# Optimization experiments

Measured on AMD Instinct MI355X. Metric: run time of the kernel, lower is better.

Reference implementation:

```python
import jax, jax.numpy as jnp
import numpy as np

NUM_LAYER = 5
N_HIDDEN = 1024
EMB_SIZE = 1024
N_CLASS = 32000
BATCH = 64
SEQ = 256


def setup_inputs() -> dict:
    key = jax.random.key(0)
    ks = jax.random.split(key, 7)
    scale = 0.02
    X = jax.random.randint(ks[0], (BATCH, SEQ), 0, N_CLASS)
    emb = jax.random.normal(ks[1], (N_CLASS, EMB_SIZE), jnp.float32) * scale
    # gate order: [i, f, o, c_tilda]; layer 0 input dim == EMB_SIZE == N_HIDDEN
    Wx = jax.random.normal(ks[2], (NUM_LAYER, 4, N_HIDDEN, N_HIDDEN), jnp.float32) * scale
    Wh = jax.random.normal(ks[3], (NUM_LAYER, 4, N_HIDDEN, N_HIDDEN), jnp.float32) * scale
    b = jnp.ones((NUM_LAYER, 4, N_HIDDEN), jnp.float32)  # original inits gate biases to ones
    W_hq = jax.random.normal(ks[4], (N_HIDDEN, N_CLASS), jnp.float32) * scale
    b_q = jnp.ones((N_CLASS,), jnp.float32)
    return {"X": X, "emb": emb, "Wx": Wx, "Wh": Wh, "b": b, "W_hq": W_hq, "b_q": b_q}


def _lstm_stack(seq, Wx, Wh, b):
    # seq: [S, B, E] time-major input
    inp = seq
    for l in range(Wx.shape[0]):  # fixed small layer count
        # precompute input-to-gate projections for all timesteps: [S, 4, B, H]
        xp = jnp.einsum('sbe,geh->sgbh', inp, Wx[l]) + b[l][:, None, :]

        def step(carry, xp_t):
            h, c = carry
            pre = xp_t + jnp.einsum('bk,gkh->gbh', h, Wh[l])  # [4, B, H]
            i = jax.nn.sigmoid(pre[0])
            f = jax.nn.sigmoid(pre[1])
            o = jax.nn.sigmoid(pre[2])
            g = jnp.tanh(pre[3])
            c = f * c + i * g
            h = o * jnp.tanh(c)
            return (h, c), h

        h0 = jnp.zeros((seq.shape[1], Wh.shape[-1]), seq.dtype)
        (_, _), hs = jax.lax.scan(step, (h0, h0), xp)
        inp = hs  # [S, B, H] feeds next layer
    return inp


def reference(X, emb, Wx, Wh, b, W_hq, b_q):
    seq = emb[X].transpose(1, 0, 2)  # [S, B, E]
    hs = _lstm_stack(seq, Wx, Wh, b)
    # output projection on the final timestep's hidden state of the top layer
    return hs[-1] @ W_hq + b_q  # [B, N_CLASS]
```

## Files before the change

kernel.cpp:

```cpp
#include <hip/hip_runtime.h>

#define SEQL 256
#define BATCH 64
#define HID 1024
#define NLAY 5
#define NCLS 32000

typedef __attribute__((__ext_vector_type__(8))) short s16x8;
typedef __attribute__((__ext_vector_type__(4))) float f32x4;

__device__ __forceinline__ unsigned short f2bf(float f) {
  unsigned u = __float_as_uint(f);
  u = u + 0x7fffu + ((u >> 16) & 1u);
  return (unsigned short)(u >> 16);
}
__device__ __forceinline__ float bf2f(unsigned short s) {
  return __uint_as_float(((unsigned)s) << 16);
}
__device__ __forceinline__ float sigm(float x) { return 1.f / (1.f + __expf(-x)); }
__device__ __forceinline__ float tanh_f(float x) {
  float a = fabsf(x);
  float e = __expf(-2.f * a);
  float t = (1.f - e) / (1.f + e);
  return x < 0.f ? -t : t;
}

__device__ __forceinline__ void llds16(const void* g, void* l) {
  __builtin_amdgcn_global_load_lds((const __attribute__((address_space(1))) unsigned int*)g,
                                   (__attribute__((address_space(3))) unsigned int*)l,
                                   16, 0, 0);
}

#define AFENCE asm volatile("" ::: "memory")
#define VW0 asm volatile("s_waitcnt vmcnt(0)" ::: "memory")
#define LW0 asm volatile("s_waitcnt lgkmcnt(0)" ::: "memory")
#define SBAR __builtin_amdgcn_s_barrier()

__global__ void pack_k(const float* __restrict__ Wx, const float* __restrict__ Wh,
                       unsigned short* __restrict__ Wp) {
  int bid = blockIdx.x;
  int k0 = bid & 63;
  int g = (bid >> 6) & 3;
  int j = (bid >> 8) & 63;
  int l = bid >> 14;
  int lane = threadIdx.x;
  int h = j * 16 + (lane & 15);
  int kb = k0 * 32 + (lane >> 4) * 8;
  const float* src;
  if (kb < 1024) src = Wx + ((size_t)((l * 4 + g) * 1024 + kb)) * 1024 + h;
  else           src = Wh + ((size_t)((l * 4 + g) * 1024 + (kb - 1024))) * 1024 + h;
  unsigned short o[8];
#pragma unroll
  for (int i = 0; i < 8; ++i) o[i] = f2bf(src[(size_t)i * 1024]);
  uint4 v;
  v.x = (unsigned)o[0] | ((unsigned)o[1] << 16);
  v.y = (unsigned)o[2] | ((unsigned)o[3] << 16);
  v.z = (unsigned)o[4] | ((unsigned)o[5] << 16);
  v.w = (unsigned)o[6] | ((unsigned)o[7] << 16);
  *(uint4*)(Wp + (((size_t)bid * 64 + lane) * 8)) = v;
}

__global__ void embed_k(const int* __restrict__ X, const float* __restrict__ emb,
                        unsigned short* __restrict__ hsA) {
  int sb = blockIdx.x;
  int t = sb >> 6, b = sb & 63;
  int row = X[b * SEQL + t];
  float4 v = ((const float4*)(emb + (size_t)row * HID))[threadIdx.x];
  unsigned short o0 = f2bf(v.x), o1 = f2bf(v.y), o2 = f2bf(v.z), o3 = f2bf(v.w);
  uint2 pk;
  pk.x = (unsigned)o0 | ((unsigned)o1 << 16);
  pk.y = (unsigned)o2 | ((unsigned)o3 << 16);
  ((uint2*)(hsA + (size_t)sb * HID))[threadIdx.x] = pk;
}

extern __shared__ char smem[];

__device__ __forceinline__ void stage16(const char* slab, char* lbuf, int srow, int sslot) {
#pragma unroll
  for (int r = 0; r < 4; ++r) {
    int rw = r * 4 + srow;
    llds16(slab + rw * 2048 + ((sslot ^ (rw & 7)) << 4), lbuf + rw * 2048 + sslot * 16);
  }
}

__device__ __forceinline__ void pollflags(const int* fl, int id, int lane) {
  if (id <= 0) return;
  for (;;) {
    int v = __hip_atomic_load(&fl[lane * 4], __ATOMIC_RELAXED, __HIP_MEMORY_SCOPE_AGENT);
    if (__all(v >= id)) break;
    __builtin_amdgcn_s_sleep(1);
  }
}

__global__ void __launch_bounds__(512, 1)
lstm_pers(const unsigned short* __restrict__ Wp, const float* __restrict__ bias,
          unsigned short* hsA, unsigned short* hsB, int* flags) {
  const int bid = blockIdx.x;
  const int bg = bid >> 6;
  const int cg = bid & 63;
  const int tid = threadIdx.x;
  const int wave = tid >> 6;
  const int lane = tid & 63;
  const int g = wave & 3;
  const int kh = wave >> 2;
  const int hl = lane & 15;
  const int ksub = lane >> 4;
  const int srow = tid >> 7;
  const int sslot = tid & 127;

  char* Bx0 = smem;
  char* Bx1 = smem + 32768;
  char* Bh = smem + 65536;
  float* pre0 = (float*)(smem + 98304);
  float* pre1 = (float*)(smem + 102656);

  int* flbg = flags + bg * 256;

  for (int l = 0; l < NLAY; ++l) {
    const unsigned short* hin = (l & 1) ? hsB : hsA;
    unsigned short* hout = (l & 1) ? hsA : hsB;
    const unsigned short* wpL =
        Wp + (size_t)(l * 64 + cg) * 131072 + (size_t)g * 32768 + (size_t)kh * 32 * 512;
    const float biasv = bias[(l * 4 + g) * 1024 + cg * 16 + hl];

    s16x8 wreg[32];
#pragma unroll
    for (int i = 0; i < 32; ++i)
      wreg[i] = *(const s16x8*)(wpL + i * 512 + lane * 8);

    float c0 = 0.f, c1 = 0.f;

    if (wave == 4) pollflags(flbg, l * 256, lane);
    AFENCE; SBAR;
#pragma unroll
    for (int r = 0; r < 4; ++r)
      ((uint4*)Bh)[r * 512 + tid] = (uint4){0u, 0u, 0u, 0u};
    stage16((const char*)hin + (size_t)(bg * 16) * 2048, Bx0, srow, sslot);
    VW0; LW0; SBAR;

    for (int t = 0; t < SEQL; ++t) {
      char* Bxp = (t & 1) ? Bx1 : Bx0;
      char* Bxn = (t & 1) ? Bx0 : Bx1;
      const bool pre_ = (t + 1 < SEQL);

      if (pre_) {
        const char* xn = (const char*)hin + ((size_t)(t + 1) * 64 + bg * 16) * 2048;
        stage16(xn, Bxn, srow, sslot);
      }

      f32x4 acc = {0.f, 0.f, 0.f, 0.f};
      if (kh == 0) {
#pragma unroll
        for (int i = 0; i < 32; ++i) {
          int off = hl * 2048 + (((i * 4 + ksub) ^ (hl & 7)) << 4);
          s16x8 a = *(const s16x8*)(Bxp + off);
          acc = __builtin_amdgcn_mfma_f32_16x16x32_bf16(a, wreg[i], acc, 0, 0, 0);
        }
#pragma unroll
        for (int r = 0; r < 4; ++r)
          pre0[(g * 16 + ksub * 4 + r) * 17 + hl] = acc[r] + biasv;
      } else if (wave == 4 && t > 0) {
        pollflags(flbg, l * 256 + t, lane);
      }
      AFENCE; SBAR;

      if (t > 0) {
        const char* hp = (const char*)hout + ((size_t)(t - 1) * 64 + bg * 16) * 2048;
        stage16(hp, Bh, srow, sslot);
      }
      VW0; SBAR;

      if (kh == 1) {
#pragma unroll
        for (int i = 0; i < 32; ++i) {
          int off = hl * 2048 + (((i * 4 + ksub) ^ (hl & 7)) << 4);
          s16x8 a = *(const s16x8*)(Bh + off);
          acc = __builtin_amdgcn_mfma_f32_16x16x32_bf16(a, wreg[i], acc, 0, 0, 0);
        }
#pragma unroll
        for (int r = 0; r < 4; ++r)
          pre1[(g * 16 + ksub * 4 + r) * 17 + hl] = acc[r];
      }
      LW0; SBAR;

      if (tid < 128) {
        int b = tid >> 3;
        int h0 = (tid & 7) * 2;
        unsigned short hw[2];
#pragma unroll
        for (int q = 0; q < 2; ++q) {
          int hh = h0 + q;
          float pi = pre0[(0 * 16 + b) * 17 + hh] + pre1[(0 * 16 + b) * 17 + hh];
          float pf = pre0[(1 * 16 + b) * 17 + hh] + pre1[(1 * 16 + b) * 17 + hh];
          float po = pre0[(2 * 16 + b) * 17 + hh] + pre1[(2 * 16 + b) * 17 + hh];
          float pg = pre0[(3 * 16 + b) * 17 + hh] + pre1[(3 * 16 + b) * 17 + hh];
          float iv = sigm(pi), fv = sigm(pf), ov = sigm(po), gv = tanh_f(pg);
          float cprev = q ? c1 : c0;
          float c = fv * cprev + iv * gv;
          if (q) c1 = c; else c0 = c;
          hw[q] = f2bf(ov * tanh_f(c));
        }
        unsigned pk = (unsigned)hw[0] | ((unsigned)hw[1] << 16);
        unsigned* dst =
            (unsigned*)(hout + ((size_t)t * 64 + bg * 16 + b) * HID + cg * 16 + h0);
        __hip_atomic_store(dst, pk, __ATOMIC_RELAXED, __HIP_MEMORY_SCOPE_AGENT);
      }
      VW0;
      SBAR;
      if (tid == 0)
        __hip_atomic_store(&flags[(bg * 64 + cg) * 4], l * 256 + t + 1, __ATOMIC_RELAXED,
                           __HIP_MEMORY_SCOPE_AGENT);
    }
  }
}

__global__ void __launch_bounds__(256) proj_k(const unsigned short* __restrict__ hlast,
                                              const float* __restrict__ Whq,
                                              float* __restrict__ part) {
  __shared__ float hlds[64 * 128];
  int kh = blockIdx.x / 125;
  int nb = blockIdx.x % 125;
  int n = nb * 256 + threadIdx.x;
  float acc[64];
#pragma unroll
  for (int b = 0; b < 64; ++b) acc[b] = 0.f;
  for (int kc = 0; kc < 4; ++kc) {
    int kbase = kh * 512 + kc * 128;
    __syncthreads();
#pragma unroll
    for (int it = 0; it < 32; ++it) {
      int id = threadIdx.x + it * 256;
      int b = id >> 7, k = id & 127;
      hlds[b * 128 + k] = bf2f(hlast[(size_t)b * HID + kbase + k]);
    }
    __syncthreads();
    for (int k4 = 0; k4 < 32; ++k4) {
      float w0 = Whq[(size_t)(kbase + k4 * 4 + 0) * NCLS + n];
      float w1 = Whq[(size_t)(kbase + k4 * 4 + 1) * NCLS + n];
      float w2 = Whq[(size_t)(kbase + k4 * 4 + 2) * NCLS + n];
      float w3 = Whq[(size_t)(kbase + k4 * 4 + 3) * NCLS + n];
#pragma unroll
      for (int b = 0; b < 64; ++b) {
        float4 h4 = *(const float4*)&hlds[b * 128 + k4 * 4];
        acc[b] += h4.x * w0 + h4.y * w1 + h4.z * w2 + h4.w * w3;
      }
    }
  }
#pragma unroll
  for (int b = 0; b < 64; ++b)
    part[(size_t)kh * 64 * NCLS + (size_t)b * NCLS + n] = acc[b];
}

__global__ void combine_k(const float* __restrict__ part, const float* __restrict__ bq,
                          float* __restrict__ out) {
  int i = blockIdx.x * 256 + threadIdx.x;
  int n = i % NCLS;
  out[i] = part[i] + part[64 * NCLS + i] + bq[n];
}

extern "C" void kernel_launch(void* const* d_in, const int* in_sizes, int n_in,
                              void* d_out, int out_size, void* d_ws, size_t ws_size,
                              hipStream_t stream) {
  const int* X = (const int*)d_in[0];
  const float* emb = (const float*)d_in[1];
  const float* Wx = (const float*)d_in[2];
  const float* Wh = (const float*)d_in[3];
  const float* bias = (const float*)d_in[4];
  const float* Whq = (const float*)d_in[5];
  const float* bq = (const float*)d_in[6];
  float* out = (float*)d_out;
  char* ws = (char*)d_ws;

  const size_t WP_OFF = 0;
  const size_t HSA_OFF = 83886080;
  const size_t HSB_OFF = HSA_OFF + 33554432;
  const size_t PART_OFF = HSB_OFF + 33554432;
  const size_t FLAG_OFF = PART_OFF + 16384000;
  const size_t NEED = FLAG_OFF + 4096;
  if (ws_size < NEED) return;

  unsigned short* Wp = (unsigned short*)(ws + WP_OFF);
  unsigned short* hsA = (unsigned short*)(ws + HSA_OFF);
  unsigned short* hsB = (unsigned short*)(ws + HSB_OFF);
  float* part = (float*)(ws + PART_OFF);
  int* flags = (int*)(ws + FLAG_OFF);

  hipMemsetAsync(flags, 0, 4096, stream);
  pack_k<<<81920, 64, 0, stream>>>(Wx, Wh, Wp);
  embed_k<<<16384, 256, 0, stream>>>(X, emb, hsA);
  (void)hipFuncSetAttribute(reinterpret_cast<const void*>(&lstm_pers),
                            hipFuncAttributeMaxDynamicSharedMemorySize, 107008);
  lstm_pers<<<256, 512, 107008, stream>>>(Wp, bias, hsA, hsB, flags);
  const unsigned short* hlastp = hsB + (size_t)255 * BATCH * HID;
  proj_k<<<250, 256, 0, stream>>>(hlastp, Whq, part);
  combine_k<<<8000, 256, 0, stream>>>(part, bq, out);
}
```

Measured before the change: 4.077 ms.

## Pipeline LSTM layers as a wavefront across blocks with ring buffers

The persistent kernel that ran the five layers in sequence, each block handling 16 batch rows, becomes a layer-wavefront kernel. Layers 0-3 run at the same time, one layer per group of 64 blocks, each block covering all 64 batch rows for 16 hidden units. Layers hand hidden states to each other through 32-slot ring buffers, with flags polled against the layer above and below. Layer 4 runs afterwards in a separate batch-split kernel that writes to an 8-slot ring. This is meant to overlap the sequential recurrences of different layers, at the cost of more staging work per block, heavier cross-block flag polling and a risk of deadlock if all blocks are not co-resident.

```diff
diff --git a/kernel.cpp b/kernel.cpp
--- a/kernel.cpp
+++ b/kernel.cpp
@@ -5,6 +5,8 @@
 #define HID 1024
 #define NLAY 5
 #define NCLS 32000
+#define RING_R 32
+#define R4 8
 
 typedef __attribute__((__ext_vector_type__(8))) short s16x8;
 typedef __attribute__((__ext_vector_type__(4))) float f32x4;
@@ -61,7 +63,7 @@
 }
 
 __global__ void embed_k(const int* __restrict__ X, const float* __restrict__ emb,
-                        unsigned short* __restrict__ hsA) {
+                        unsigned short* __restrict__ x0) {
   int sb = blockIdx.x;
   int t = sb >> 6, b = sb & 63;
   int row = X[b * SEQL + t];
@@ -70,10 +72,152 @@
   uint2 pk;
   pk.x = (unsigned)o0 | ((unsigned)o1 << 16);
   pk.y = (unsigned)o2 | ((unsigned)o3 << 16);
-  ((uint2*)(hsA + (size_t)sb * HID))[threadIdx.x] = pk;
+  ((uint2*)(x0 + (size_t)sb * HID))[threadIdx.x] = pk;
 }
 
 extern __shared__ char smem[];
+
+
+__device__ __forceinline__ void stageAB(const char* slab, char* AB, int tid) {
+#pragma unroll
+  for (int it = 0; it < 16; ++it) {
+    int c = tid + it * 512;
+    int row = c >> 7, slot = c & 127;
+    llds16(slab + row * 2048 + ((slot ^ (row & 7)) << 4), AB + row * 2048 + slot * 16);
+  }
+}
+
+__device__ __forceinline__ void mfma128(const char* AB, const s16x8* wreg, int hl,
+                                        int ksub, f32x4 (&acc)[4]) {
+  const int sw = hl & 7;
+#pragma unroll
+  for (int i = 0; i < 32; ++i) {
+    int so = ((i * 4 + ksub) ^ sw) << 4;
+#pragma unroll
+    for (int m = 0; m < 4; ++m) {
+      s16x8 a = *(const s16x8*)(AB + (m * 16 + hl) * 2048 + so);
+      acc[m] = __builtin_amdgcn_mfma_f32_16x16x32_bf16(a, wreg[i], acc[m], 0, 0, 0);
+    }
+  }
+}
+
+__device__ __forceinline__ void pollA(const int* fl, int l, int t, int lane) {
+  for (;;) {
+    bool ok = true;
+    int own = __hip_atomic_load(&fl[(l * 64 + lane) * 4], __ATOMIC_RELAXED, __HIP_MEMORY_SCOPE_AGENT);
+    ok &= (own >= t);
+    if (l > 0) {
+      int up = __hip_atomic_load(&fl[((l - 1) * 64 + lane) * 4], __ATOMIC_RELAXED, __HIP_MEMORY_SCOPE_AGENT);
+      ok &= (up >= t + 1);
+    }
+    if (l < 3) {
+      int dn = __hip_atomic_load(&fl[((l + 1) * 64 + lane) * 4], __ATOMIC_RELAXED, __HIP_MEMORY_SCOPE_AGENT);
+      ok &= (dn >= t - (RING_R - 1));
+    }
+    if (__all(ok)) break;
+    __builtin_amdgcn_s_sleep(1);
+  }
+}
+
+__global__ void __launch_bounds__(512) __attribute__((amdgpu_waves_per_eu(2, 2)))
+lstm_wave(const unsigned short* __restrict__ Wp, const float* __restrict__ bias,
+          const unsigned short* __restrict__ x0, unsigned short* ring,
+          unsigned short* hs3, int* flags) {
+  const int l = blockIdx.x >> 6;
+  const int cg = blockIdx.x & 63;
+  const int tid = threadIdx.x;
+  const int wave = tid >> 6;
+  const int lane = tid & 63;
+  const int g = wave & 3;
+  const int kh = wave >> 2;
+  const int hl = lane & 15;
+  const int ksub = lane >> 4;
+  char* AB = smem;
+  float* pre = (float*)(smem + 131072);
+
+  const unsigned short* wpL =
+      Wp + (size_t)(l * 64 + cg) * 131072 + (size_t)g * 32768 + (size_t)kh * 16384;
+  const float biasv = bias[(l * 4 + g) * 1024 + cg * 16 + hl];
+
+  s16x8 wreg[32];
+#pragma unroll
+  for (int i = 0; i < 32; ++i) wreg[i] = *(const s16x8*)(wpL + i * 512 + lane * 8);
+
+  float c0 = 0.f, c1 = 0.f;
+  const int gb = tid >> 3;
+  const int gh = (tid & 7) * 2;
+
+  for (int t = 0; t < SEQL; ++t) {
+    if (wave == 0) pollA(flags, l, t, lane);
+    AFENCE; SBAR;
+
+    const char* xs = (l == 0)
+        ? (const char*)x0 + (size_t)t * 131072
+        : (const char*)ring + ((size_t)((l - 1) * RING_R + (t & (RING_R - 1)))) * 131072;
+    stageAB(xs, AB, tid);
+    VW0; SBAR;
+
+    f32x4 acc[4];
+#pragma unroll
+    for (int m = 0; m < 4; ++m) acc[m] = (f32x4){0.f, 0.f, 0.f, 0.f};
+    if (kh == 0) {
+      mfma128(AB, wreg, hl, ksub, acc);
+#pragma unroll
+      for (int m = 0; m < 4; ++m)
+#pragma unroll
+        for (int r = 0; r < 4; ++r)
+          pre[(g * 64 + m * 16 + ksub * 4 + r) * 17 + hl] = acc[m][r] + biasv;
+    }
+    LW0; SBAR;
+
+    if (t > 0) {
+      const char* hsrc = (l == 3)
+          ? (const char*)hs3 + (size_t)(t - 1) * 131072
+          : (const char*)ring + ((size_t)(l * RING_R + ((t - 1) & (RING_R - 1)))) * 131072;
+      stageAB(hsrc, AB, tid);
+    }
+    VW0; SBAR;
+
+    if (kh == 1 && t > 0) {
+      mfma128(AB, wreg, hl, ksub, acc);
+#pragma unroll
+      for (int m = 0; m < 4; ++m)
+#pragma unroll
+        for (int r = 0; r < 4; ++r)
+          pre[(g * 64 + m * 16 + ksub * 4 + r) * 17 + hl] += acc[m][r];
+    }
+    LW0; SBAR;
+
+    {
+      unsigned short hw[2];
+#pragma unroll
+      for (int q = 0; q < 2; ++q) {
+        int hh = gh + q;
+        float pi = pre[(0 * 64 + gb) * 17 + hh];
+        float pf = pre[(1 * 64 + gb) * 17 + hh];
+        float po = pre[(2 * 64 + gb) * 17 + hh];
+        float pg = pre[(3 * 64 + gb) * 17 + hh];
+        float iv = sigm(pi), fv = sigm(pf), ov = sigm(po), gv = tanh_f(pg);
+        float cprev = q ? c1 : c0;
+        float c = fv * cprev + iv * gv;
+        if (q) c1 = c; else c0 = c;
+        hw[q] = f2bf(ov * tanh_f(c));
+      }
+      unsigned pk = (unsigned)hw[0] | ((unsigned)hw[1] << 16);
+      unsigned short* dstbase = (l == 3)
+          ? hs3 + (size_t)t * 65536
+          : ring + ((size_t)(l * RING_R + (t & (RING_R - 1)))) * 65536;
+      unsigned* dst = (unsigned*)(dstbase + (size_t)gb * 1024 + cg * 16 + gh);
+      __hip_atomic_store(dst, pk, __ATOMIC_RELAXED, __HIP_MEMORY_SCOPE_AGENT);
+    }
+    VW0;
+    SBAR;
+    if (tid == 0)
+      __hip_atomic_store(&flags[(l * 64 + cg) * 4], t + 1, __ATOMIC_RELAXED,
+                         __HIP_MEMORY_SCOPE_AGENT);
+  }
+}
+
 
 __device__ __forceinline__ void stage16(const char* slab, char* lbuf, int srow, int sslot) {
 #pragma unroll
@@ -83,7 +227,7 @@
   }
 }
 
-__device__ __forceinline__ void pollflags(const int* fl, int id, int lane) {
+__device__ __forceinline__ void pollB(const int* fl, int id, int lane) {
   if (id <= 0) return;
   for (;;) {
     int v = __hip_atomic_load(&fl[lane * 4], __ATOMIC_RELAXED, __HIP_MEMORY_SCOPE_AGENT);
@@ -92,12 +236,11 @@
   }
 }
 
-__global__ void __launch_bounds__(512, 1)
-lstm_pers(const unsigned short* __restrict__ Wp, const float* __restrict__ bias,
-          unsigned short* hsA, unsigned short* hsB, int* flags) {
-  const int bid = blockIdx.x;
-  const int bg = bid >> 6;
-  const int cg = bid & 63;
+__global__ void __launch_bounds__(512) __attribute__((amdgpu_waves_per_eu(2, 2)))
+lstm_last(const unsigned short* __restrict__ Wp, const float* __restrict__ bias,
+          const unsigned short* __restrict__ hs3, unsigned short* h4, int* flagsB) {
+  const int bg = blockIdx.x >> 6;
+  const int cg = blockIdx.x & 63;
   const int tid = threadIdx.x;
   const int wave = tid >> 6;
   const int lane = tid & 63;
@@ -114,103 +257,96 @@
   float* pre0 = (float*)(smem + 98304);
   float* pre1 = (float*)(smem + 102656);
 
-  int* flbg = flags + bg * 256;
-
-  for (int l = 0; l < NLAY; ++l) {
-    const unsigned short* hin = (l & 1) ? hsB : hsA;
-    unsigned short* hout = (l & 1) ? hsA : hsB;
-    const unsigned short* wpL =
-        Wp + (size_t)(l * 64 + cg) * 131072 + (size_t)g * 32768 + (size_t)kh * 32 * 512;
-    const float biasv = bias[(l * 4 + g) * 1024 + cg * 16 + hl];
-
-    s16x8 wreg[32];
-#pragma unroll
-    for (int i = 0; i < 32; ++i)
-      wreg[i] = *(const s16x8*)(wpL + i * 512 + lane * 8);
-
-    float c0 = 0.f, c1 = 0.f;
-
-    if (wave == 4) pollflags(flbg, l * 256, lane);
+  int* flbg = flagsB + bg * 256;
+
+  const unsigned short* wpL =
+      Wp + (size_t)(4 * 64 + cg) * 131072 + (size_t)g * 32768 + (size_t)kh * 16384;
+  const float biasv = bias[(4 * 4 + g) * 1024 + cg * 16 + hl];
+
+  s16x8 wreg[32];
+#pragma unroll
+  for (int i = 0; i < 32; ++i) wreg[i] = *(const s16x8*)(wpL + i * 512 + lane * 8);
+
+  float c0 = 0.f, c1 = 0.f;
+
+#pragma unroll
+  for (int r = 0; r < 4; ++r)
+    ((uint4*)Bh)[r * 512 + tid] = (uint4){0u, 0u, 0u, 0u};
+  stage16((const char*)hs3 + (size_t)(bg * 16) * 2048, Bx0, srow, sslot);
+  VW0; LW0; SBAR;
+
+  for (int t = 0; t < SEQL; ++t) {
+    char* Bxp = (t & 1) ? Bx1 : Bx0;
+    char* Bxn = (t & 1) ? Bx0 : Bx1;
+    const bool pre_ = (t + 1 < SEQL);
+
+    if (pre_) {
+      const char* xn = (const char*)hs3 + ((size_t)(t + 1) * 64 + bg * 16) * 2048;
+      stage16(xn, Bxn, srow, sslot);
+    }
+
+    f32x4 acc = {0.f, 0.f, 0.f, 0.f};
+    if (kh == 0) {
+#pragma unroll
+      for (int i = 0; i < 32; ++i) {
+        int off = hl * 2048 + (((i * 4 + ksub) ^ (hl & 7)) << 4);
+        s16x8 a = *(const s16x8*)(Bxp + off);
+        acc = __builtin_amdgcn_mfma_f32_16x16x32_bf16(a, wreg[i], acc, 0, 0, 0);
+      }
+#pragma unroll
+      for (int r = 0; r < 4; ++r)
+        pre0[(g * 16 + ksub * 4 + r) * 17 + hl] = acc[r] + biasv;
+    } else if (wave == 4 && t > 0) {
+      pollB(flbg, t, lane);
+    }
     AFENCE; SBAR;
-#pragma unroll
-    for (int r = 0; r < 4; ++r)
-      ((uint4*)Bh)[r * 512 + tid] = (uint4){0u, 0u, 0u, 0u};
-    stage16((const char*)hin + (size_t)(bg * 16) * 2048, Bx0, srow, sslot);
-    VW0; LW0; SBAR;
-
-    for (int t = 0; t < SEQL; ++t) {
-      char* Bxp = (t & 1) ? Bx1 : Bx0;
-      char* Bxn = (t & 1) ? Bx0 : Bx1;
-      const bool pre_ = (t + 1 < SEQL);
-
-      if (pre_) {
-        const char* xn = (const char*)hin + ((size_t)(t + 1) * 64 + bg * 16) * 2048;
-        stage16(xn, Bxn, srow, sslot);
+
+    if (t > 0) {
+      const char* hp = (const char*)h4 + ((size_t)((t - 1) & (R4 - 1)) * 64 + bg * 16) * 2048;
+      stage16(hp, Bh, srow, sslot);
+    }
+    VW0; SBAR;
+
+    if (kh == 1) {
+#pragma unroll
+      for (int i = 0; i < 32; ++i) {
+        int off = hl * 2048 + (((i * 4 + ksub) ^ (hl & 7)) << 4);
+        s16x8 a = *(const s16x8*)(Bh + off);
+        acc = __builtin_amdgcn_mfma_f32_16x16x32_bf16(a, wreg[i], acc, 0, 0, 0);
       }
-
-      f32x4 acc = {0.f, 0.f, 0.f, 0.f};
-      if (kh == 0) {
-#pragma unroll
-        for (int i = 0; i < 32; ++i) {
-          int off = hl * 2048 + (((i * 4 + ksub) ^ (hl & 7)) << 4);
-          s16x8 a = *(const s16x8*)(Bxp + off);
-          acc = __builtin_amdgcn_mfma_f32_16x16x32_bf16(a, wreg[i], acc, 0, 0, 0);
-        }
-#pragma unroll
-        for (int r = 0; r < 4; ++r)
-          pre0[(g * 16 + ksub * 4 + r) * 17 + hl] = acc[r] + biasv;
-      } else if (wave == 4 && t > 0) {
-        pollflags(flbg, l * 256 + t, lane);
+#pragma unroll
+      for (int r = 0; r < 4; ++r)
+        pre1[(g * 16 + ksub * 4 + r) * 17 + hl] = acc[r];
+    }
+    LW0; SBAR;
+
+    if (tid < 128) {
+      int b = tid >> 3;
+      int h0 = (tid & 7) * 2;
+      unsigned short hw[2];
+#pragma unroll
+      for (int q = 0; q < 2; ++q) {
+        int hh = h0 + q;
+        float pi = pre0[(0 * 16 + b) * 17 + hh] + pre1[(0 * 16 + b) * 17 + hh];
+        float pf = pre0[(1 * 16 + b) * 17 + hh] + pre1[(1 * 16 + b) * 17 + hh];
+        float po = pre0[(2 * 16 + b) * 17 + hh] + pre1[(2 * 16 + b) * 17 + hh];
+        float pg = pre0[(3 * 16 + b) * 17 + hh] + pre1[(3 * 16 + b) * 17 + hh];
+        float iv = sigm(pi), fv = sigm(pf), ov = sigm(po), gv = tanh_f(pg);
+        float cprev = q ? c1 : c0;
+        float c = fv * cprev + iv * gv;
+        if (q) c1 = c; else c0 = c;
+        hw[q] = f2bf(ov * tanh_f(c));
       }
-      AFENCE; SBAR;
-
-      if (t > 0) {
-        const char* hp = (const char*)hout + ((size_t)(t - 1) * 64 + bg * 16) * 2048;
-        stage16(hp, Bh, srow, sslot);
-      }
-      VW0; SBAR;
-
-      if (kh == 1) {
-#pragma unroll
-        for (int i = 0; i < 32; ++i) {
-          int off = hl * 2048 + (((i * 4 + ksub) ^ (hl & 7)) << 4);
-          s16x8 a = *(const s16x8*)(Bh + off);
-          acc = __builtin_amdgcn_mfma_f32_16x16x32_bf16(a, wreg[i], acc, 0, 0, 0);
-        }
-#pragma unroll
-        for (int r = 0; r < 4; ++r)
-          pre1[(g * 16 + ksub * 4 + r) * 17 + hl] = acc[r];
-      }
-      LW0; SBAR;
-
-      if (tid < 128) {
-        int b = tid >> 3;
-        int h0 = (tid & 7) * 2;
-        unsigned short hw[2];
-#pragma unroll
-        for (int q = 0; q < 2; ++q) {
-          int hh = h0 + q;
-          float pi = pre0[(0 * 16 + b) * 17 + hh] + pre1[(0 * 16 + b) * 17 + hh];
-          float pf = pre0[(1 * 16 + b) * 17 + hh] + pre1[(1 * 16 + b) * 17 + hh];
-          float po = pre0[(2 * 16 + b) * 17 + hh] + pre1[(2 * 16 + b) * 17 + hh];
-          float pg = pre0[(3 * 16 + b) * 17 + hh] + pre1[(3 * 16 + b) * 17 + hh];
-          float iv = sigm(pi), fv = sigm(pf), ov = sigm(po), gv = tanh_f(pg);
-          float cprev = q ? c1 : c0;
-          float c = fv * cprev + iv * gv;
-          if (q) c1 = c; else c0 = c;
-          hw[q] = f2bf(ov * tanh_f(c));
-        }
-        unsigned pk = (unsigned)hw[0] | ((unsigned)hw[1] << 16);
-        unsigned* dst =
-            (unsigned*)(hout + ((size_t)t * 64 + bg * 16 + b) * HID + cg * 16 + h0);
-        __hip_atomic_store(dst, pk, __ATOMIC_RELAXED, __HIP_MEMORY_SCOPE_AGENT);
-      }
-      VW0;
-      SBAR;
-      if (tid == 0)
-        __hip_atomic_store(&flags[(bg * 64 + cg) * 4], l * 256 + t + 1, __ATOMIC_RELAXED,
-                           __HIP_MEMORY_SCOPE_AGENT);
-    }
+      unsigned pk = (unsigned)hw[0] | ((unsigned)hw[1] << 16);
+      unsigned* dst = (unsigned*)(h4 + ((size_t)(t & (R4 - 1)) * 64 + bg * 16 + b) * 1024 +
+                                  cg * 16 + h0);
+      __hip_atomic_store(dst, pk, __ATOMIC_RELAXED, __HIP_MEMORY_SCOPE_AGENT);
+    }
+    VW0;
+    SBAR;
+    if (tid == 0)
+      __hip_atomic_store(&flagsB[(bg * 64 + cg) * 4], t + 1, __ATOMIC_RELAXED,
+                         __HIP_MEMORY_SCOPE_AGENT);
   }
 }
 
@@ -241,8 +377,8 @@
       float w3 = Whq[(size_t)(kbase + k4 * 4 + 3) * NCLS + n];
 #pragma unroll
       for (int b = 0; b < 64; ++b) {
-        float4 h4 = *(const float4*)&hlds[b * 128 + k4 * 4];
-        acc[b] += h4.x * w0 + h4.y * w1 + h4.z * w2 + h4.w * w3;
+        float4 h4v = *(const float4*)&hlds[b * 128 + k4 * 4];
+        acc[b] += h4v.x * w0 + h4v.y * w1 + h4v.z * w2 + h4v.w * w3;
       }
     }
   }
@@ -272,26 +408,32 @@
   char* ws = (char*)d_ws;
 
   const size_t WP_OFF = 0;
-  const size_t HSA_OFF = 83886080;
-  const size_t HSB_OFF = HSA_OFF + 33554432;
-  const size_t PART_OFF = HSB_OFF + 33554432;
-  const size_t FLAG_OFF = PART_OFF + 16384000;
-  const size_t NEED = FLAG_OFF + 4096;
+  const size_t X0_OFF = 83886080;
+  const size_t RING_OFF = X0_OFF + 33554432;
+  const size_t HS3_OFF = RING_OFF + 3u * RING_R * 131072;
+  const size_t H4_OFF = HS3_OFF + 33554432;
+  const size_t FLAG_OFF = H4_OFF + (size_t)R4 * 131072;
+  const size_t NEED = FLAG_OFF + 8192;
   if (ws_size < NEED) return;
 
   unsigned short* Wp = (unsigned short*)(ws + WP_OFF);
-  unsigned short* hsA = (unsigned short*)(ws + HSA_OFF);
-  unsigned short* hsB = (unsigned short*)(ws + HSB_OFF);
-  float* part = (float*)(ws + PART_OFF);
+  unsigned short* x0 = (unsigned short*)(ws + X0_OFF);
+  unsigned short* ring = (unsigned short*)(ws + RING_OFF);
+  unsigned short* hs3 = (unsigned short*)(ws + HS3_OFF);
+  unsigned short* h4 = (unsigned short*)(ws + H4_OFF);
   int* flags = (int*)(ws + FLAG_OFF);
-
-  hipMemsetAsync(flags, 0, 4096, stream);
+  float* part = (float*)(ws + X0_OFF);
+
+  hipMemsetAsync(flags, 0, 8192, stream);
   pack_k<<<81920, 64, 0, stream>>>(Wx, Wh, Wp);
-  embed_k<<<16384, 256, 0, stream>>>(X, emb, hsA);
-  (void)hipFuncSetAttribute(reinterpret_cast<const void*>(&lstm_pers),
+  embed_k<<<16384, 256, 0, stream>>>(X, emb, x0);
+  (void)hipFuncSetAttribute(reinterpret_cast<const void*>(&lstm_wave),
+                            hipFuncAttributeMaxDynamicSharedMemorySize, 148480);
+  (void)hipFuncSetAttribute(reinterpret_cast<const void*>(&lstm_last),
                             hipFuncAttributeMaxDynamicSharedMemorySize, 107008);
-  lstm_pers<<<256, 512, 107008, stream>>>(Wp, bias, hsA, hsB, flags);
-  const unsigned short* hlastp = hsB + (size_t)255 * BATCH * HID;
+  lstm_wave<<<256, 512, 148480, stream>>>(Wp, bias, x0, ring, hs3, flags);
+  lstm_last<<<256, 512, 107008, stream>>>(Wp, bias, hs3, h4, flags + 1024);
+  const unsigned short* hlastp = h4 + (size_t)(R4 - 1) * 64 * 1024;
   proj_k<<<250, 256, 0, stream>>>(hlastp, Whq, part);
   combine_k<<<8000, 256, 0, stream>>>(part, bq, out);
 }
```

New measurement: 12.31 ms. +201.9%, slower.

## Split x-path and h-path waves into independent roles with fewer barriers per step

Applied to the files above, without the earlier changes.

Reorganises the per-timestep schedule of the persistent LSTM kernel so that waves 0-3 alone stage and multiply the input projection, while waves 4-7 alone poll the flags, stage the previous hidden state and run the recurrent MFMAs at raised priority. This cuts the per-step block barriers from four to two and takes the x-path work off the recurrent critical path. The MFMA chain is split into two independent accumulators to shorten dependency stalls, and the launch bound moves to waves_per_eu(2) with asm keep-alive on the weight registers. Risks are register pressure or spills under the new occupancy hint, and subtle ordering hazards from the reduced waits and barriers.

```diff
diff --git a/kernel.cpp b/kernel.cpp
--- a/kernel.cpp
+++ b/kernel.cpp
@@ -35,6 +35,7 @@
 #define VW0 asm volatile("s_waitcnt vmcnt(0)" ::: "memory")
 #define LW0 asm volatile("s_waitcnt lgkmcnt(0)" ::: "memory")
 #define SBAR __builtin_amdgcn_s_barrier()
+#define KEEPV(x) asm volatile("" : "+v"(x))
 
 __global__ void pack_k(const float* __restrict__ Wx, const float* __restrict__ Wh,
                        unsigned short* __restrict__ Wp) {
@@ -75,12 +76,30 @@
 
 extern __shared__ char smem[];
 
-__device__ __forceinline__ void stage16(const char* slab, char* lbuf, int srow, int sslot) {
-#pragma unroll
-  for (int r = 0; r < 4; ++r) {
-    int rw = r * 4 + srow;
-    llds16(slab + rw * 2048 + ((sslot ^ (rw & 7)) << 4), lbuf + rw * 2048 + sslot * 16);
-  }
+__device__ __forceinline__ void stageG(const char* slab, char* lbuf, int wq, int lane) {
+#pragma unroll
+  for (int it = 0; it < 8; ++it) {
+    int chunk = wq + it * 4;
+    int row = chunk >> 1;
+    int slot = (chunk & 1) * 64 + lane;
+    llds16(slab + row * 2048 + ((slot ^ (row & 7)) << 4),
+           lbuf + row * 2048 + slot * 16);
+  }
+}
+
+__device__ __forceinline__ f32x4 mf32(const char* buf, const s16x8* wreg, int hl, int ksub) {
+  f32x4 aA = {0.f, 0.f, 0.f, 0.f};
+  f32x4 aB = {0.f, 0.f, 0.f, 0.f};
+  const char* ab = buf + hl * 2048;
+  const int sw = hl & 7;
+#pragma unroll
+  for (int i = 0; i < 16; ++i) {
+    s16x8 a0 = *(const s16x8*)(ab + ((((2 * i) * 4 + ksub) ^ sw) << 4));
+    aA = __builtin_amdgcn_mfma_f32_16x16x32_bf16(a0, wreg[2 * i], aA, 0, 0, 0);
+    s16x8 a1 = *(const s16x8*)(ab + ((((2 * i + 1) * 4 + ksub) ^ sw) << 4));
+    aB = __builtin_amdgcn_mfma_f32_16x16x32_bf16(a1, wreg[2 * i + 1], aB, 0, 0, 0);
+  }
+  return aA + aB;
 }
 
 __device__ __forceinline__ void pollflags(const int* fl, int id, int lane) {
@@ -92,7 +111,7 @@
   }
 }
 
-__global__ void __launch_bounds__(512, 1)
+__global__ void __launch_bounds__(512) __attribute__((amdgpu_waves_per_eu(2)))
 lstm_pers(const unsigned short* __restrict__ Wp, const float* __restrict__ bias,
           unsigned short* hsA, unsigned short* hsB, int* flags) {
   const int bid = blockIdx.x;
@@ -103,10 +122,9 @@
   const int lane = tid & 63;
   const int g = wave & 3;
   const int kh = wave >> 2;
+  const int wq = wave & 3;
   const int hl = lane & 15;
   const int ksub = lane >> 4;
-  const int srow = tid >> 7;
-  const int sslot = tid & 127;
 
   char* Bx0 = smem;
   char* Bx1 = smem + 32768;
@@ -120,68 +138,58 @@
     const unsigned short* hin = (l & 1) ? hsB : hsA;
     unsigned short* hout = (l & 1) ? hsA : hsB;
     const unsigned short* wpL =
-        Wp + (size_t)(l * 64 + cg) * 131072 + (size_t)g * 32768 + (size_t)kh * 32 * 512;
+        Wp + (size_t)(l * 64 + cg) * 131072 + (size_t)g * 32768 + (size_t)kh * 16384;
     const float biasv = bias[(l * 4 + g) * 1024 + cg * 16 + hl];
 
     s16x8 wreg[32];
 #pragma unroll
-    for (int i = 0; i < 32; ++i)
-      wreg[i] = *(const s16x8*)(wpL + i * 512 + lane * 8);
+    for (int i = 0; i < 32; ++i) wreg[i] = *(const s16x8*)(wpL + i * 512 + lane * 8);
+#pragma unroll
+    for (int i = 0; i < 32; ++i) KEEPV(wreg[i]);
 
     float c0 = 0.f, c1 = 0.f;
 
-    if (wave == 4) pollflags(flbg, l * 256, lane);
+    if (kh == 1) pollflags(flbg, l * 256, lane);
     AFENCE; SBAR;
-#pragma unroll
-    for (int r = 0; r < 4; ++r)
-      ((uint4*)Bh)[r * 512 + tid] = (uint4){0u, 0u, 0u, 0u};
-    stage16((const char*)hin + (size_t)(bg * 16) * 2048, Bx0, srow, sslot);
-    VW0; LW0; SBAR;
+    if (kh == 0) { stageG((const char*)hin + (size_t)(bg * 16) * 2048, Bx0, wq, lane); VW0; }
+    SBAR;
 
     for (int t = 0; t < SEQL; ++t) {
       char* Bxp = (t & 1) ? Bx1 : Bx0;
       char* Bxn = (t & 1) ? Bx0 : Bx1;
       const bool pre_ = (t + 1 < SEQL);
 
-      if (pre_) {
-        const char* xn = (const char*)hin + ((size_t)(t + 1) * 64 + bg * 16) * 2048;
-        stage16(xn, Bxn, srow, sslot);
-      }
-
-      f32x4 acc = {0.f, 0.f, 0.f, 0.f};
       if (kh == 0) {
-#pragma unroll
-        for (int i = 0; i < 32; ++i) {
-          int off = hl * 2048 + (((i * 4 + ksub) ^ (hl & 7)) << 4);
-          s16x8 a = *(const s16x8*)(Bxp + off);
-          acc = __builtin_amdgcn_mfma_f32_16x16x32_bf16(a, wreg[i], acc, 0, 0, 0);
+        if (pre_) {
+          const char* xn = (const char*)hin + ((size_t)(t + 1) * 64 + bg * 16) * 2048;
+          stageG(xn, Bxn, wq, lane);
         }
+        f32x4 acc = mf32(Bxp, wreg, hl, ksub);
 #pragma unroll
         for (int r = 0; r < 4; ++r)
           pre0[(g * 16 + ksub * 4 + r) * 17 + hl] = acc[r] + biasv;
-      } else if (wave == 4 && t > 0) {
-        pollflags(flbg, l * 256 + t, lane);
+        LW0;
+      } else {
+        __builtin_amdgcn_s_setprio(1);
+        if (t > 0) {
+          pollflags(flbg, l * 256 + t, lane);
+          AFENCE;
+          const char* hp = (const char*)hout + ((size_t)(t - 1) * 64 + bg * 16) * 2048;
+          stageG(hp, Bh, wq, lane);
+          VW0;
+          f32x4 acc = mf32(Bh, wreg, hl, ksub);
+#pragma unroll
+          for (int r = 0; r < 4; ++r)
+            pre1[(g * 16 + ksub * 4 + r) * 17 + hl] = acc[r];
+        } else {
+#pragma unroll
+          for (int r = 0; r < 4; ++r)
+            pre1[(g * 16 + ksub * 4 + r) * 17 + hl] = 0.f;
+        }
+        __builtin_amdgcn_s_setprio(0);
+        LW0;
       }
-      AFENCE; SBAR;
-
-      if (t > 0) {
-        const char* hp = (const char*)hout + ((size_t)(t - 1) * 64 + bg * 16) * 2048;
-        stage16(hp, Bh, srow, sslot);
-      }
-      VW0; SBAR;
-
-      if (kh == 1) {
-#pragma unroll
-        for (int i = 0; i < 32; ++i) {
-          int off = hl * 2048 + (((i * 4 + ksub) ^ (hl & 7)) << 4);
-          s16x8 a = *(const s16x8*)(Bh + off);
-          acc = __builtin_amdgcn_mfma_f32_16x16x32_bf16(a, wreg[i], acc, 0, 0, 0);
-        }
-#pragma unroll
-        for (int r = 0; r < 4; ++r)
-          pre1[(g * 16 + ksub * 4 + r) * 17 + hl] = acc[r];
-      }
-      LW0; SBAR;
+      SBAR;
 
       if (tid < 128) {
         int b = tid >> 3;
@@ -205,7 +213,7 @@
             (unsigned*)(hout + ((size_t)t * 64 + bg * 16 + b) * HID + cg * 16 + h0);
         __hip_atomic_store(dst, pk, __ATOMIC_RELAXED, __HIP_MEMORY_SCOPE_AGENT);
       }
-      VW0;
+      if (kh == 0) VW0;
       SBAR;
       if (tid == 0)
         __hip_atomic_store(&flags[(bg * 64 + cg) * 4], l * 256 + t + 1, __ATOMIC_RELAXED,
```

After: 6.356 ms. +55.9%, slower.
